# Performance work log

Hardware: AMD Instinct MI355X
Metric: run time of the kernel (lower is better)

## Reference

```python
import jax, jax.numpy as jnp
import numpy as np

N, C = 16384, 4096
MARGIN = 0.1


def setup_inputs() -> dict:
    key = jax.random.key(0)
    k1, k2 = jax.random.split(key)
    cossim = jax.random.normal(k1, (N, C), dtype=jnp.float32)
    correct = jax.random.randint(k2, (N,), 0, C)
    target = jax.nn.one_hot(correct, C, dtype=jnp.int32)  # one-hot [N, C]
    return {"cossim": cossim, "target": target}


def reference(cossim, target):
    # correct column per row (target is one-hot)
    correct_idx = jnp.argmax(target, axis=1)  # [N]
    correct_sim = jnp.take_along_axis(cossim, correct_idx[:, None], axis=1)  # [N, 1]
    # hinge = clamp(margin + sim - correct_sim, min=0), excluding the correct column
    hinge = jnp.maximum(MARGIN + cossim - correct_sim, 0.0)  # [N, C]
    is_correct = target == 1
    hinge = jnp.where(is_correct, 0.0, hinge)
    loss = jnp.sum(hinge) / N
    return loss
```

## Files before the change

kernel.cpp:

```cpp
#include <hip/hip_runtime.h>

#define N_ROWS 16384
#define N_COLS 4096
#define MARGIN 0.1f
#define BLOCK  256
#define NBLK   2048
#define ROWS_PER_BLK (N_ROWS / NBLK)
#define V4_PER_ROW (N_COLS / 4)
#define K_LOADS (V4_PER_ROW / BLOCK)

typedef float vf4 __attribute__((ext_vector_type(4)));
typedef int   vi4 __attribute__((ext_vector_type(4)));

__global__ __launch_bounds__(BLOCK) void
mm_fused_kernel(const float* __restrict__ cossim,
                const int* __restrict__ target,
                float* __restrict__ partials) {
    const vf4* __restrict__ c4 = (const vf4*)cossim;
    const vi4* __restrict__ t4 = (const vi4*)target;

    __shared__ float s_wave[2][BLOCK / 64];
    const int lane = threadIdx.x & 63, wave = threadIdx.x >> 6;

    float acc = 0.0f;
    const unsigned row0 = blockIdx.x * ROWS_PER_BLK;

#pragma unroll
    for (int r = 0; r < ROWS_PER_BLK; ++r) {
        const unsigned rbase = (row0 + r) * V4_PER_ROW + threadIdx.x;

        vf4 c[K_LOADS];
#pragma unroll
        for (int k = 0; k < K_LOADS; ++k)
            c[k] = __builtin_nontemporal_load(&c4[rbase + k * BLOCK]);
        vi4 t[K_LOADS];
#pragma unroll
        for (int k = 0; k < K_LOADS; ++k)
            t[k] = __builtin_nontemporal_load(&t4[rbase + k * BLOCK]);

        float s = 0.0f;
#pragma unroll
        for (int k = 0; k < K_LOADS; ++k)
#pragma unroll
            for (int j = 0; j < 4; ++j)
                s += (t[k][j] != 0) ? c[k][j] : 0.0f;

#pragma unroll
        for (int off = 32; off > 0; off >>= 1)
            s += __shfl_down(s, off, 64);
        if (lane == 0) s_wave[r & 1][wave] = s;
        __syncthreads();
        const float srow = s_wave[r & 1][0] + s_wave[r & 1][1]
                         + s_wave[r & 1][2] + s_wave[r & 1][3];

        const float mc = MARGIN - srow;
#pragma unroll
        for (int k = 0; k < K_LOADS; ++k)
#pragma unroll
            for (int j = 0; j < 4; ++j)
                acc += fmaxf(mc + c[k][j], 0.0f);
    }

#pragma unroll
    for (int off = 32; off > 0; off >>= 1)
        acc += __shfl_down(acc, off, 64);
    __shared__ float s_acc[BLOCK / 64];
    if (lane == 0) s_acc[wave] = acc;
    __syncthreads();
    if (threadIdx.x == 0)
        partials[blockIdx.x] = s_acc[0] + s_acc[1] + s_acc[2] + s_acc[3];
}

__global__ __launch_bounds__(BLOCK) void
mm_reduce_kernel(const float* __restrict__ partials, float* __restrict__ out) {
    const int t = threadIdx.x;
    float acc = 0.0f;
    for (int i = t; i < NBLK; i += BLOCK) acc += partials[i];
#pragma unroll
    for (int off = 32; off > 0; off >>= 1)
        acc += __shfl_down(acc, off, 64);
    __shared__ float s_wave[BLOCK / 64];
    const int lane = t & 63, wave = t >> 6;
    if (lane == 0) s_wave[wave] = acc;
    __syncthreads();
    if (t == 0)
        out[0] = (s_wave[0] + s_wave[1] + s_wave[2] + s_wave[3]) * (1.0f / N_ROWS)
                 - MARGIN;
}

extern "C" void kernel_launch(void* const* d_in, const int* in_sizes, int n_in,
                              void* d_out, int out_size, void* d_ws, size_t ws_size,
                              hipStream_t stream) {
    const float* cossim = (const float*)d_in[0];
    const int*   target = (const int*)d_in[1];
    float* out      = (float*)d_out;
    float* partials = (float*)d_ws;

    mm_fused_kernel<<<NBLK, BLOCK, 0, stream>>>(cossim, target, partials);
    mm_reduce_kernel<<<1, BLOCK, 0, stream>>>(partials, out);
}
```

Before: 471.1 us.

## Assign whole rows to single wavefronts and drop block-level syncs

Each wavefront now processes two full rows on its own, so the per-row correct-score reduction becomes an xor-shuffle butterfly with no shared memory and no __syncthreads. The target loads are issued in groups of four interleaved with the selection to cut register pressure, and launch_bounds requests 4 blocks per SM. In exchange each lane holds 16 float4 values per row, which raises VGPR use and may reduce occupancy or memory-level parallelism.

After: 466.7 us. About the same (-0.9%).

```diff
diff --git a/kernel.cpp b/kernel.cpp
--- a/kernel.cpp
+++ b/kernel.cpp
@@ -4,56 +4,54 @@
 #define N_COLS 4096
 #define MARGIN 0.1f
 #define BLOCK  256
-#define NBLK   2048
-#define ROWS_PER_BLK (N_ROWS / NBLK)
+#define WAVES_PER_BLK (BLOCK / 64)
+#define ROWS_PER_WAVE 2
+#define NBLK   (N_ROWS / (WAVES_PER_BLK * ROWS_PER_WAVE))
 #define V4_PER_ROW (N_COLS / 4)
-#define K_LOADS (V4_PER_ROW / BLOCK)
+#define K_LOADS (V4_PER_ROW / 64)
 
 typedef float vf4 __attribute__((ext_vector_type(4)));
 typedef int   vi4 __attribute__((ext_vector_type(4)));
 
-__global__ __launch_bounds__(BLOCK) void
+__global__ __launch_bounds__(BLOCK, 4) void
 mm_fused_kernel(const float* __restrict__ cossim,
                 const int* __restrict__ target,
                 float* __restrict__ partials) {
     const vf4* __restrict__ c4 = (const vf4*)cossim;
     const vi4* __restrict__ t4 = (const vi4*)target;
-
-    __shared__ float s_wave[2][BLOCK / 64];
     const int lane = threadIdx.x & 63, wave = threadIdx.x >> 6;
+    const unsigned gwave = blockIdx.x * WAVES_PER_BLK + wave;
 
     float acc = 0.0f;
-    const unsigned row0 = blockIdx.x * ROWS_PER_BLK;
-
 #pragma unroll
-    for (int r = 0; r < ROWS_PER_BLK; ++r) {
-        const unsigned rbase = (row0 + r) * V4_PER_ROW + threadIdx.x;
+    for (int r = 0; r < ROWS_PER_WAVE; ++r) {
+        const unsigned row  = gwave * ROWS_PER_WAVE + r;
+        const unsigned base = row * V4_PER_ROW + lane;
 
         vf4 c[K_LOADS];
 #pragma unroll
         for (int k = 0; k < K_LOADS; ++k)
-            c[k] = __builtin_nontemporal_load(&c4[rbase + k * BLOCK]);
-        vi4 t[K_LOADS];
-#pragma unroll
-        for (int k = 0; k < K_LOADS; ++k)
-            t[k] = __builtin_nontemporal_load(&t4[rbase + k * BLOCK]);
+            c[k] = __builtin_nontemporal_load(&c4[base + k * 64]);
 
         float s = 0.0f;
 #pragma unroll
-        for (int k = 0; k < K_LOADS; ++k)
+        for (int g = 0; g < K_LOADS / 4; ++g) {
+            vi4 t[4];
 #pragma unroll
-            for (int j = 0; j < 4; ++j)
-                s += (t[k][j] != 0) ? c[k][j] : 0.0f;
+            for (int u = 0; u < 4; ++u)
+                t[u] = __builtin_nontemporal_load(&t4[base + (g * 4 + u) * 64]);
+#pragma unroll
+            for (int u = 0; u < 4; ++u)
+#pragma unroll
+                for (int j = 0; j < 4; ++j)
+                    s += (t[u][j] != 0) ? c[g * 4 + u][j] : 0.0f;
+        }
 
 #pragma unroll
-        for (int off = 32; off > 0; off >>= 1)
-            s += __shfl_down(s, off, 64);
-        if (lane == 0) s_wave[r & 1][wave] = s;
-        __syncthreads();
-        const float srow = s_wave[r & 1][0] + s_wave[r & 1][1]
-                         + s_wave[r & 1][2] + s_wave[r & 1][3];
+        for (int off = 1; off < 64; off <<= 1)
+            s += __shfl_xor(s, off, 64);
 
-        const float mc = MARGIN - srow;
+        const float mc = MARGIN - s;
 #pragma unroll
         for (int k = 0; k < K_LOADS; ++k)
 #pragma unroll
@@ -64,7 +62,7 @@
 #pragma unroll
     for (int off = 32; off > 0; off >>= 1)
         acc += __shfl_down(acc, off, 64);
-    __shared__ float s_acc[BLOCK / 64];
+    __shared__ float s_acc[WAVES_PER_BLK];
     if (lane == 0) s_acc[wave] = acc;
     __syncthreads();
     if (threadIdx.x == 0)
```
